# Kernel tuning notes

Measured on AMD Instinct MI355X. Metric: run time of the kernel, lower is better.

Reference implementation:

```python
import jax, jax.numpy as jnp
import numpy as np

ALPHA, GAMMA = 0.25, 2.0
EPS_CLS, EPS_DICE = 1e-8, 1e-5


def box_cxcywh_to_xyxy(b):
    cx, cy, w, h = b[..., 0], b[..., 1], b[..., 2], b[..., 3]
    return jnp.stack([cx - 0.5 * w, cy - 0.5 * h, cx + 0.5 * w, cy + 0.5 * h], axis=-1)


def generalized_box_iou(b1, b2):
    # b1: [N,4], b2: [T,4] in xyxy -> [N,T]
    area1 = (b1[:, 2] - b1[:, 0]) * (b1[:, 3] - b1[:, 1])
    area2 = (b2[:, 2] - b2[:, 0]) * (b2[:, 3] - b2[:, 1])
    lt = jnp.maximum(b1[:, None, :2], b2[None, :, :2])
    rb = jnp.minimum(b1[:, None, 2:], b2[None, :, 2:])
    wh = jnp.clip(rb - lt, 0.0)
    inter = wh[..., 0] * wh[..., 1]
    union = area1[:, None] + area2[None, :] - inter
    iou = inter / union
    lt_e = jnp.minimum(b1[:, None, :2], b2[None, :, :2])
    rb_e = jnp.maximum(b1[:, None, 2:], b2[None, :, 2:])
    wh_e = jnp.clip(rb_e - lt_e, 0.0)
    area_e = wh_e[..., 0] * wh_e[..., 1]
    return iou - (area_e - union) / area_e


def masks_to_boxes(masks):
    # DETR util: masks [N,H,W] (any float; nonzero treated as 'on') -> xyxy [N,4]
    n, h, w = masks.shape
    x = jnp.arange(w, dtype=masks.dtype)
    y = jnp.arange(h, dtype=masks.dtype)
    nz = masks != 0
    x_mask = masks * x[None, None, :]
    x_max = x_mask.reshape(n, -1).max(-1)
    x_min = jnp.where(nz, x_mask, 1e8).reshape(n, -1).min(-1)
    y_mask = masks * y[None, :, None]
    y_max = y_mask.reshape(n, -1).max(-1)
    y_min = jnp.where(nz, y_mask, 1e8).reshape(n, -1).min(-1)
    return jnp.stack([x_min, y_min, x_max, y_max], axis=1)


def setup_inputs() -> dict:
    key = jax.random.key(0)
    k1, k2, k3, k4, k5, k6 = jax.random.split(key, 6)
    return {
        'pred_logits': jax.random.normal(k1, (2, 300, 91), dtype=jnp.float32),
        'pred_boxes': jax.random.uniform(k2, (2, 300, 4), dtype=jnp.float32),
        'pred_masks': jax.random.normal(k3, (2, 300, 256, 256), dtype=jnp.float32),
        'tgt_boxes': jax.random.uniform(k4, (60, 4), dtype=jnp.float32),
        'tgt_ids': jax.random.randint(k5, (60,), 0, 91, dtype=jnp.int64) if jax.config.jax_enable_x64 else jax.random.randint(k5, (60,), 0, 91).astype(jnp.int32),
        'tgt_masks': jax.random.randint(k6, (60, 256, 256), 0, 2, dtype=jnp.int32),
    }


def reference(pred_logits, pred_boxes, pred_masks, tgt_boxes, tgt_ids, tgt_masks):
    bs, Q, C = pred_logits.shape
    N = bs * Q
    tgt_masks_f = tgt_masks.astype(pred_masks.dtype)

    # --- focal classification cost ---
    out_prob = jax.nn.sigmoid(pred_logits.reshape(N, C))
    neg_cc = (1 - ALPHA) * out_prob ** GAMMA * -jnp.log(1 - out_prob + EPS_CLS)
    pos_cc = ALPHA * (1 - out_prob) ** GAMMA * -jnp.log(out_prob + EPS_CLS)
    cost_class = pos_cc[:, tgt_ids] - neg_cc[:, tgt_ids]  # [N,T]

    # --- L1 box cost (cdist p=1) ---
    out_bbox = pred_boxes.reshape(N, 4)
    cost_bbox = jnp.abs(out_bbox[:, None, :] - tgt_boxes[None, :, :]).sum(-1)

    # --- GIoU box cost ---
    cost_giou = -generalized_box_iou(box_cxcywh_to_xyxy(out_bbox),
                                     box_cxcywh_to_xyxy(tgt_boxes))

    # --- GIoU on mask-derived boxes (faithful to original, incl. cxcywh conversion) ---
    out_mask = pred_masks.reshape(N, pred_masks.shape[2], pred_masks.shape[3])
    cost_giou_m2b = -generalized_box_iou(
        box_cxcywh_to_xyxy(masks_to_boxes(out_mask)),
        box_cxcywh_to_xyxy(masks_to_boxes(tgt_masks_f)))

    # --- pairwise dice cost: batched matmul instead of the O(N*T) python loop ---
    HW = out_mask.shape[1] * out_mask.shape[2]
    p = jax.nn.sigmoid(out_mask).reshape(N, HW)      # [N,HW]
    t = tgt_masks_f.reshape(tgt_masks_f.shape[0], HW)  # [T,HW] binary
    inter = p @ t.T                                   # [N,T]
    union = p.sum(1)[:, None] + t.sum(1)[None, :]
    cost_mask_dice = 1.0 - (2 * inter + EPS_DICE) / (union + EPS_DICE)

    # --- pairwise focal cost; exact closed form for binary targets:
    # focal(i,j) = mean_px[ t*pos_px + (1-t)*neg_px ]
    pos_px = ALPHA * (1 - p) ** GAMMA * -jnp.log(p)
    neg_px = (1 - ALPHA) * p ** GAMMA * -jnp.log(1 - p)
    cost_mask_focal = (pos_px @ t.T + neg_px.sum(1)[:, None] - neg_px @ t.T) / HW

    Cmat = (cost_bbox + cost_class + cost_giou +
            cost_giou_m2b + cost_mask_dice + cost_mask_focal)
    return Cmat.reshape(bs, Q, -1)
```

## Files before the change

### kernel.cpp

```cpp
#include <hip/hip_runtime.h>
#include <math.h>

#define HW    65536
#define TNUM  60
#define NPRED 600
#define NCLS  91
#define PS    32
#define NTIL  38

typedef float f32x4 __attribute__((ext_vector_type(4)));
typedef short s16x8 __attribute__((ext_vector_type(8)));

__global__ void hm_tgt_stats(const int* __restrict__ tm, float* __restrict__ tstat) {
    int j = blockIdx.x >> 3, chunk = blockIdx.x & 7;
    int tid = threadIdx.x;
    const int* row = tm + (size_t)j * HW + chunk * 8192;
    float cnt = 0.f, xmax = -INFINITY, ymax = -INFINITY, xmin = INFINITY, ymin = INFINITY;
    for (int i = tid; i < 8192; i += 256) {
        int pix = chunk * 8192 + i;
        float t = (float)row[i];
        float xf = (float)(pix & 255), yf = (float)(pix >> 8);
        float xm = t * xf, ym = t * yf;
        cnt += t;
        xmax = fmaxf(xmax, xm); ymax = fmaxf(ymax, ym);
        bool nz = (t != 0.f);
        xmin = fminf(xmin, nz ? xm : 1e8f);
        ymin = fminf(ymin, nz ? ym : 1e8f);
    }
#pragma unroll
    for (int o = 1; o < 64; o <<= 1) {
        cnt += __shfl_xor(cnt, o);
        xmax = fmaxf(xmax, __shfl_xor(xmax, o));
        ymax = fmaxf(ymax, __shfl_xor(ymax, o));
        xmin = fminf(xmin, __shfl_xor(xmin, o));
        ymin = fminf(ymin, __shfl_xor(ymin, o));
    }
    __shared__ float s[5][4];
    int w = tid >> 6;
    if ((tid & 63) == 0) { s[0][w]=cnt; s[1][w]=xmin; s[2][w]=ymin; s[3][w]=xmax; s[4][w]=ymax; }
    __syncthreads();
    if (tid == 0) {
        float* o = tstat + (size_t)(j * 8 + chunk) * 5;
        o[0] = s[0][0]+s[0][1]+s[0][2]+s[0][3];
        o[1] = fminf(fminf(s[1][0],s[1][1]),fminf(s[1][2],s[1][3]));
        o[2] = fminf(fminf(s[2][0],s[2][1]),fminf(s[2][2],s[2][3]));
        o[3] = fmaxf(fmaxf(s[3][0],s[3][1]),fmaxf(s[3][2],s[3][3]));
        o[4] = fmaxf(fmaxf(s[4][0],s[4][1]),fmaxf(s[4][2],s[4][3]));
    }
}

__global__ void hm_build_tpack(const int* __restrict__ tm, unsigned short* __restrict__ tp) {
    int bid = blockIdx.x;
    int j = bid >> 8, chunk = bid & 255;
    int pix = chunk * 256 + threadIdx.x;
    unsigned short v = 0;
    if (j < TNUM) v = (tm[(size_t)j * HW + pix] != 0) ? (unsigned short)0x3F80 : (unsigned short)0;
    size_t idx = ((size_t)(pix >> 5) * 64 + j) * 32 + (size_t)((pix >> 3) & 3) * 8 + (pix & 7);
    tp[idx] = v;
}

__device__ inline void pix_proc(float x, int e, float xfb, float yf,
                                __bf16* P, __bf16* F,
                                float& sp, float& sn,
                                float& xM, float& yM, float& xm, float& ym) {
    float ex = __expf(x);
    float opex = 1.f + ex;
    float p = __fdividef(ex, opex);
    float spx = __logf(opex);
    float spmx = spx - x;
    float om = 1.f - p;
    float pos = (om * om) * (0.25f * spmx);
    float neg = (p * p) * (0.75f * spx);
    sp += p; sn += neg;
    float xf = xfb + (float)e;
    float xmsk = x * xf, ymsk = x * yf;
    xM = fmaxf(xM, xmsk); yM = fmaxf(yM, ymsk);
    bool nz = (x != 0.f);
    xm = fminf(xm, nz ? xmsk : 1e8f);
    ym = fminf(ym, nz ? ymsk : 1e8f);
    P[e] = (__bf16)p;
    F[e] = (__bf16)(pos - neg);
}

__launch_bounds__(256, 4)
__global__ void hm_heavy(const float* __restrict__ pm, const unsigned short* __restrict__ tp,
                         float* __restrict__ dots, float* __restrict__ stats) {
    int id = blockIdx.x;
    int xcd = id & 7, q = id >> 3;
    int ntile = q % NTIL, ps = xcd + 8 * (q / NTIL);
    int bl = ntile * PS + ps;
    int tid = threadIdx.x, w = tid >> 6, l = tid & 63, g = l >> 4, c = l & 15;
    int n0 = ntile * 16;
    int row = min(n0 + c, NPRED - 1);
    const float* A = pm + (size_t)row * HW;
    const s16x8* tpv = (const s16x8*)tp;
    int pb = ps * 2048 + w * 512;

    f32x4 acc[4][2];
#pragma unroll
    for (int nt = 0; nt < 4; ++nt)
#pragma unroll
        for (int m = 0; m < 2; ++m) acc[nt][m] = (f32x4)0.f;

    float sp = 0.f, sn = 0.f;
    float xM = -INFINITY, yM = -INFINITY, xm = INFINITY, ym = INFINITY;

#pragma unroll 2
    for (int step = 0; step < 16; ++step) {
        int k0 = pb + step * 32;
        int kk = k0 + g * 8;
        float4 aa = *(const float4*)(A + kk);
        float4 ab = *(const float4*)(A + kk + 4);
        float yf = (float)(kk >> 8);
        float xfb = (float)(kk & 255);

        union { __bf16 h[8]; s16x8 v; } P, F;
        float x[8] = {aa.x, aa.y, aa.z, aa.w, ab.x, ab.y, ab.z, ab.w};
#pragma unroll
        for (int e = 0; e < 8; ++e)
            pix_proc(x[e], e, xfb, yf, P.h, F.h, sp, sn, xM, yM, xm, ym);

        int bbase = (k0 >> 5) * 256 + c * 4 + g;
#pragma unroll
        for (int nt = 0; nt < 4; ++nt) {
            s16x8 bf = tpv[bbase + nt * 64];
            acc[nt][0] = __builtin_amdgcn_mfma_f32_16x16x32_bf16(P.v, bf, acc[nt][0], 0, 0, 0);
            acc[nt][1] = __builtin_amdgcn_mfma_f32_16x16x32_bf16(F.v, bf, acc[nt][1], 0, 0, 0);
        }
    }

#pragma unroll
    for (int o = 16; o <= 32; o <<= 1) {
        sp += __shfl_xor(sp, o); sn += __shfl_xor(sn, o);
        xM = fmaxf(xM, __shfl_xor(xM, o)); yM = fmaxf(yM, __shfl_xor(yM, o));
        xm = fminf(xm, __shfl_xor(xm, o)); ym = fminf(ym, __shfl_xor(ym, o));
    }
    if (l < 16) {
        float* so = stats + ((size_t)((bl * 4 + w) * 16 + l)) * 6;
        so[0] = sp; so[1] = sn; so[2] = xM; so[3] = yM; so[4] = xm; so[5] = ym;
    }

    __shared__ float ldsD[4][32][64];
#pragma unroll
    for (int nt = 0; nt < 4; ++nt)
#pragma unroll
        for (int m = 0; m < 2; ++m)
#pragma unroll
            for (int r = 0; r < 4; ++r)
                ldsD[w][(nt * 2 + m) * 4 + r][l] = acc[nt][m][r];
    __syncthreads();

    for (int idx = tid; idx < 2048; idx += 256) {
        int mat = idx >> 10, rl = (idx >> 6) & 15, col = idx & 63;
        int gg = rl >> 2, rg = rl & 3;
        int nt = col >> 4, cc = col & 15;
        int lane = gg * 16 + cc;
        int off = (nt * 2 + mat) * 4 + rg;
        float s = ldsD[0][off][lane] + ldsD[1][off][lane] + ldsD[2][off][lane] + ldsD[3][off][lane];
        dots[(size_t)bl * 2048 + idx] = s;
    }
}

__global__ void hm_pred_reduce(const float* __restrict__ stats, float* __restrict__ pstat) {
    int n = blockIdx.x;
    int l = threadIdx.x;
    int ntile = n >> 4, r = n & 15;
    const float* s0 = stats + ((size_t)(ntile * 128 + l) * 16 + r) * 6;
    const float* s1 = stats + ((size_t)(ntile * 128 + l + 64) * 16 + r) * 6;
    float v0 = s0[0] + s1[0];
    float v1 = s0[1] + s1[1];
    float v2 = fmaxf(s0[2], s1[2]);
    float v3 = fmaxf(s0[3], s1[3]);
    float v4 = fminf(s0[4], s1[4]);
    float v5 = fminf(s0[5], s1[5]);
#pragma unroll
    for (int o = 1; o < 64; o <<= 1) {
        v0 += __shfl_xor(v0, o); v1 += __shfl_xor(v1, o);
        v2 = fmaxf(v2, __shfl_xor(v2, o)); v3 = fmaxf(v3, __shfl_xor(v3, o));
        v4 = fminf(v4, __shfl_xor(v4, o)); v5 = fminf(v5, __shfl_xor(v5, o));
    }
    if (l == 0) {
        float* o = pstat + (size_t)n * 6;
        o[0] = v0; o[1] = v1; o[2] = v2; o[3] = v3; o[4] = v4; o[5] = v5;
    }
}

__device__ inline float giou2(float ax0, float ay0, float ax1, float ay1,
                              float bx0, float by0, float bx1, float by1) {
    float area1 = (ax1 - ax0) * (ay1 - ay0);
    float area2 = (bx1 - bx0) * (by1 - by0);
    float ltx = fmaxf(ax0, bx0), lty = fmaxf(ay0, by0);
    float rbx = fminf(ax1, bx1), rby = fminf(ay1, by1);
    float iw = fmaxf(rbx - ltx, 0.f), ih = fmaxf(rby - lty, 0.f);
    float inter = iw * ih;
    float uni = area1 + area2 - inter;
    float iou = inter / uni;
    float ex0 = fminf(ax0, bx0), ey0 = fminf(ay0, by0);
    float ex1 = fmaxf(ax1, bx1), ey1 = fmaxf(ay1, by1);
    float ew = fmaxf(ex1 - ex0, 0.f), eh = fmaxf(ey1 - ey0, 0.f);
    float ae = ew * eh;
    return iou - (ae - uni) / ae;
}

__device__ inline float giou_cxcywh(float acx, float acy, float aw, float ah,
                                    float bcx, float bcy, float bw, float bh) {
    return giou2(acx - 0.5f * aw, acy - 0.5f * ah, acx + 0.5f * aw, acy + 0.5f * ah,
                 bcx - 0.5f * bw, bcy - 0.5f * bh, bcx + 0.5f * bw, bcy + 0.5f * bh);
}

__global__ void hm_combine(const float* __restrict__ pred_logits,
                           const float* __restrict__ pred_boxes,
                           const float* __restrict__ tgt_boxes,
                           const int* __restrict__ tgt_ids,
                           const float* __restrict__ dots,
                           const float* __restrict__ pstat,
                           const float* __restrict__ tstat,
                           float* __restrict__ out) {
    int idx = blockIdx.x * blockDim.x + threadIdx.x;
    if (idx >= NPRED * TNUM) return;
    int n = idx / TNUM, j = idx % TNUM;
    int ntile = n >> 4, r = n & 15;

    const float* db = dots + (size_t)ntile * PS * 2048 + r * 64 + j;
    float dp = 0.f, df = 0.f;
#pragma unroll
    for (int ps = 0; ps < PS; ++ps) {
        dp += db[ps * 2048];
        df += db[ps * 2048 + 1024];
    }

    float tcnt = 0.f, txm = INFINITY, tym = INFINITY, txM = -INFINITY, tyM = -INFINITY;
#pragma unroll
    for (int k = 0; k < 8; ++k) {
        const float* tb = tstat + (size_t)(j * 8 + k) * 5;
        tcnt += tb[0];
        txm = fminf(txm, tb[1]); tym = fminf(tym, tb[2]);
        txM = fmaxf(txM, tb[3]); tyM = fmaxf(tyM, tb[4]);
    }

    const float* pp = pstat + (size_t)n * 6;
    float sum_p = pp[0], sum_neg = pp[1];
    float pxM = pp[2], pyM = pp[3], pxm = pp[4], pym = pp[5];

    float4 ob = ((const float4*)pred_boxes)[n];
    float4 tb4 = ((const float4*)tgt_boxes)[j];
    float cbbox = fabsf(ob.x - tb4.x) + fabsf(ob.y - tb4.y) + fabsf(ob.z - tb4.z) + fabsf(ob.w - tb4.w);

    float cgiou = -giou_cxcywh(ob.x, ob.y, ob.z, ob.w, tb4.x, tb4.y, tb4.z, tb4.w);

    int id = tgt_ids[j];
    float lg = pred_logits[(size_t)n * NCLS + id];
    float e = __expf(lg);
    float pr = __fdividef(e, 1.f + e);
    float poscc = 0.25f * (1.f - pr) * (1.f - pr) * (-__logf(pr + 1e-8f));
    float negcc = 0.75f * pr * pr * (-__logf(1.f - pr + 1e-8f));
    float cclass = poscc - negcc;

    float cm2b = -giou_cxcywh(pxm, pym, pxM, pyM, txm, tym, txM, tyM);

    float un = sum_p + tcnt;
    float cdice = 1.f - (2.f * dp + 1e-5f) / (un + 1e-5f);

    float cfocal = (df + sum_neg) * (1.0f / (float)HW);

    out[idx] = cbbox + cclass + cgiou + cm2b + cdice + cfocal;
}

extern "C" void kernel_launch(void* const* d_in, const int* in_sizes, int n_in,
                              void* d_out, int out_size, void* d_ws, size_t ws_size,
                              hipStream_t stream) {
    const float* pred_logits = (const float*)d_in[0];
    const float* pred_boxes  = (const float*)d_in[1];
    const float* pred_masks  = (const float*)d_in[2];
    const float* tgt_boxes   = (const float*)d_in[3];
    const int*   tgt_ids     = (const int*)d_in[4];
    const int*   tgt_masks   = (const int*)d_in[5];
    float* out = (float*)d_out;

    char* wsb = (char*)d_ws;
    unsigned short* tpack = (unsigned short*)wsb;
    float* dots  = (float*)(wsb + 8388608);
    float* stats = (float*)(wsb + 18350080);
    float* pstat = (float*)(wsb + 20217856);
    float* tstat = (float*)(wsb + 20232256);

    hipLaunchKernelGGL(hm_tgt_stats, dim3(TNUM * 8), dim3(256), 0, stream, tgt_masks, tstat);
    hipLaunchKernelGGL(hm_build_tpack, dim3(64 * 256), dim3(256), 0, stream, tgt_masks, tpack);
    hipLaunchKernelGGL(hm_heavy, dim3(NTIL * PS), dim3(256), 0, stream, pred_masks, tpack, dots, stats);
    hipLaunchKernelGGL(hm_pred_reduce, dim3(NPRED), dim3(64), 0, stream, stats, pstat);
    hipLaunchKernelGGL(hm_combine, dim3((NPRED * TNUM + 255) / 256), dim3(256), 0, stream,
                       pred_logits, pred_boxes, tgt_boxes, tgt_ids, dots, pstat, tstat, out);
}
```

Before: 94.07 us.

## Split heavy kernel per-wave over K, drop LDS reduction, store partial dots in fp16

The heavy kernel is restructured so each 128-thread block holds two waves working on different 16-row tiles, and each wave owns its own 512-pixel K slice (128 slices instead of 32). This removes the in-block LDS cross-wave reduction and its __syncthreads. Partial dot products are written directly as packed half2 (dice and focal together). The combine kernel now sums 128 partials per output instead of 32. This trades LDS traffic and sync for more partial-sum memory traffic, and fp16 storage of partial sums loses precision.

```diff
diff --git a/kernel.cpp b/kernel.cpp
--- a/kernel.cpp
+++ b/kernel.cpp
@@ -1,12 +1,13 @@
 #include <hip/hip_runtime.h>
+#include <hip/hip_fp16.h>
 #include <math.h>
 
 #define HW    65536
 #define TNUM  60
 #define NPRED 600
 #define NCLS  91
-#define PS    32
-#define NTIL  38
+#define PS    128
+#define RTP   20
 
 typedef float f32x4 __attribute__((ext_vector_type(4)));
 typedef short s16x8 __attribute__((ext_vector_type(8)));
@@ -82,19 +83,19 @@
     F[e] = (__bf16)(pos - neg);
 }
 
-__launch_bounds__(256, 4)
+__launch_bounds__(128, 8)
 __global__ void hm_heavy(const float* __restrict__ pm, const unsigned short* __restrict__ tp,
-                         float* __restrict__ dots, float* __restrict__ stats) {
+                         __half2* __restrict__ dots, float* __restrict__ stats) {
     int id = blockIdx.x;
     int xcd = id & 7, q = id >> 3;
-    int ntile = q % NTIL, ps = xcd + 8 * (q / NTIL);
-    int bl = ntile * PS + ps;
+    int rtp = q % RTP, psg = q / RTP;
+    int ps = xcd + 8 * psg;
     int tid = threadIdx.x, w = tid >> 6, l = tid & 63, g = l >> 4, c = l & 15;
-    int n0 = ntile * 16;
-    int row = min(n0 + c, NPRED - 1);
+    int rt = rtp * 2 + w;
+    int row = min(rt * 16 + c, NPRED - 1);
     const float* A = pm + (size_t)row * HW;
     const s16x8* tpv = (const s16x8*)tp;
-    int pb = ps * 2048 + w * 512;
+    int pb = ps * 512;
 
     f32x4 acc[4][2];
 #pragma unroll
@@ -136,37 +137,28 @@
         xm = fminf(xm, __shfl_xor(xm, o)); ym = fminf(ym, __shfl_xor(ym, o));
     }
     if (l < 16) {
-        float* so = stats + ((size_t)((bl * 4 + w) * 16 + l)) * 6;
+        float* so = stats + ((size_t)(rt * PS + ps) * 16 + l) * 6;
         so[0] = sp; so[1] = sn; so[2] = xM; so[3] = yM; so[4] = xm; so[5] = ym;
     }
 
-    __shared__ float ldsD[4][32][64];
+    size_t dbase = (size_t)(rt * PS + ps) * 1024;
 #pragma unroll
     for (int nt = 0; nt < 4; ++nt)
 #pragma unroll
-        for (int m = 0; m < 2; ++m)
-#pragma unroll
-            for (int r = 0; r < 4; ++r)
-                ldsD[w][(nt * 2 + m) * 4 + r][l] = acc[nt][m][r];
-    __syncthreads();
-
-    for (int idx = tid; idx < 2048; idx += 256) {
-        int mat = idx >> 10, rl = (idx >> 6) & 15, col = idx & 63;
-        int gg = rl >> 2, rg = rl & 3;
-        int nt = col >> 4, cc = col & 15;
-        int lane = gg * 16 + cc;
-        int off = (nt * 2 + mat) * 4 + rg;
-        float s = ldsD[0][off][lane] + ldsD[1][off][lane] + ldsD[2][off][lane] + ldsD[3][off][lane];
-        dots[(size_t)bl * 2048 + idx] = s;
-    }
+        for (int r = 0; r < 4; ++r) {
+            __half2 h;
+            h.x = __float2half_rn(acc[nt][0][r]);
+            h.y = __float2half_rn(acc[nt][1][r]);
+            dots[dbase + (size_t)((g * 4 + r) * 64 + nt * 16 + c)] = h;
+        }
 }
 
 __global__ void hm_pred_reduce(const float* __restrict__ stats, float* __restrict__ pstat) {
     int n = blockIdx.x;
     int l = threadIdx.x;
-    int ntile = n >> 4, r = n & 15;
-    const float* s0 = stats + ((size_t)(ntile * 128 + l) * 16 + r) * 6;
-    const float* s1 = stats + ((size_t)(ntile * 128 + l + 64) * 16 + r) * 6;
+    int rt = n >> 4, r = n & 15;
+    const float* s0 = stats + ((size_t)(rt * PS + l) * 16 + r) * 6;
+    const float* s1 = stats + ((size_t)(rt * PS + l + 64) * 16 + r) * 6;
     float v0 = s0[0] + s1[0];
     float v1 = s0[1] + s1[1];
     float v2 = fmaxf(s0[2], s1[2]);
@@ -212,21 +204,22 @@
                            const float* __restrict__ pred_boxes,
                            const float* __restrict__ tgt_boxes,
                            const int* __restrict__ tgt_ids,
-                           const float* __restrict__ dots,
+                           const __half2* __restrict__ dots,
                            const float* __restrict__ pstat,
                            const float* __restrict__ tstat,
                            float* __restrict__ out) {
     int idx = blockIdx.x * blockDim.x + threadIdx.x;
     if (idx >= NPRED * TNUM) return;
     int n = idx / TNUM, j = idx % TNUM;
-    int ntile = n >> 4, r = n & 15;
-
-    const float* db = dots + (size_t)ntile * PS * 2048 + r * 64 + j;
+    int rt = n >> 4, r = n & 15;
+
+    const __half2* db = dots + (size_t)rt * PS * 1024 + r * 64 + j;
     float dp = 0.f, df = 0.f;
-#pragma unroll
+#pragma unroll 8
     for (int ps = 0; ps < PS; ++ps) {
-        dp += db[ps * 2048];
-        df += db[ps * 2048 + 1024];
+        __half2 v = db[(size_t)ps * 1024];
+        dp += __half2float(v.x);
+        df += __half2float(v.y);
     }
 
     float tcnt = 0.f, txm = INFINITY, tym = INFINITY, txM = -INFINITY, tyM = -INFINITY;
@@ -279,14 +272,14 @@
 
     char* wsb = (char*)d_ws;
     unsigned short* tpack = (unsigned short*)wsb;
-    float* dots  = (float*)(wsb + 8388608);
-    float* stats = (float*)(wsb + 18350080);
-    float* pstat = (float*)(wsb + 20217856);
-    float* tstat = (float*)(wsb + 20232256);
+    __half2* dots = (__half2*)(wsb + 8388608);
+    float* stats  = (float*)(wsb + 29360128);
+    float* pstat  = (float*)(wsb + 31326208);
+    float* tstat  = (float*)(wsb + 31340608);
 
     hipLaunchKernelGGL(hm_tgt_stats, dim3(TNUM * 8), dim3(256), 0, stream, tgt_masks, tstat);
     hipLaunchKernelGGL(hm_build_tpack, dim3(64 * 256), dim3(256), 0, stream, tgt_masks, tpack);
-    hipLaunchKernelGGL(hm_heavy, dim3(NTIL * PS), dim3(256), 0, stream, pred_masks, tpack, dots, stats);
+    hipLaunchKernelGGL(hm_heavy, dim3(RTP * PS), dim3(128), 0, stream, pred_masks, tpack, dots, stats);
     hipLaunchKernelGGL(hm_pred_reduce, dim3(NPRED), dim3(64), 0, stream, stats, pstat);
     hipLaunchKernelGGL(hm_combine, dim3((NPRED * TNUM + 255) / 256), dim3(256), 0, stream,
                        pred_logits, pred_boxes, tgt_boxes, tgt_ids, dots, pstat, tstat, out);
```

Result: slower. 335.2 us (+256.3%).

## Double split-K partitions, raise occupancy, reduce heavy-kernel stats in-block

Applied to the files above, without the earlier changes.

Splits the pixel dimension into twice as many partitions, so each block handles half as many pixels and twice as many blocks are launched. Launch bounds rise to 6 waves-groups per CU, and the LDS staging buffer is halved by reducing the two accumulator matrices one after the other. Per-wave stats are now combined inside the block, and the sigmoid's divide is replaced by a hardware reciprocal. The cost is twice as many partial dot-product results written to and read back from global memory, plus a few extra barriers.

```diff
diff --git a/kernel.cpp b/kernel.cpp
--- a/kernel.cpp
+++ b/kernel.cpp
@@ -5,7 +5,7 @@
 #define TNUM  60
 #define NPRED 600
 #define NCLS  91
-#define PS    32
+#define PS    64
 #define NTIL  38
 
 typedef float f32x4 __attribute__((ext_vector_type(4)));
@@ -65,10 +65,10 @@
                                 float& xM, float& yM, float& xm, float& ym) {
     float ex = __expf(x);
     float opex = 1.f + ex;
-    float p = __fdividef(ex, opex);
+    float om = __builtin_amdgcn_rcpf(opex);
+    float p = 1.f - om;
     float spx = __logf(opex);
     float spmx = spx - x;
-    float om = 1.f - p;
     float pos = (om * om) * (0.25f * spmx);
     float neg = (p * p) * (0.75f * spx);
     sp += p; sn += neg;
@@ -82,19 +82,20 @@
     F[e] = (__bf16)(pos - neg);
 }
 
-__launch_bounds__(256, 4)
+__launch_bounds__(256, 6)
 __global__ void hm_heavy(const float* __restrict__ pm, const unsigned short* __restrict__ tp,
                          float* __restrict__ dots, float* __restrict__ stats) {
     int id = blockIdx.x;
     int xcd = id & 7, q = id >> 3;
-    int ntile = q % NTIL, ps = xcd + 8 * (q / NTIL);
+    int ntile = q % NTIL, psg = q / NTIL;
+    int ps = xcd + 8 * psg;
     int bl = ntile * PS + ps;
     int tid = threadIdx.x, w = tid >> 6, l = tid & 63, g = l >> 4, c = l & 15;
     int n0 = ntile * 16;
     int row = min(n0 + c, NPRED - 1);
     const float* A = pm + (size_t)row * HW;
     const s16x8* tpv = (const s16x8*)tp;
-    int pb = ps * 2048 + w * 512;
+    int pb = ps * 1024 + w * 256;
 
     f32x4 acc[4][2];
 #pragma unroll
@@ -106,7 +107,7 @@
     float xM = -INFINITY, yM = -INFINITY, xm = INFINITY, ym = INFINITY;
 
 #pragma unroll 2
-    for (int step = 0; step < 16; ++step) {
+    for (int step = 0; step < 8; ++step) {
         int k0 = pb + step * 32;
         int kk = k0 + g * 8;
         float4 aa = *(const float4*)(A + kk);
@@ -135,29 +136,55 @@
         xM = fmaxf(xM, __shfl_xor(xM, o)); yM = fmaxf(yM, __shfl_xor(yM, o));
         xm = fminf(xm, __shfl_xor(xm, o)); ym = fminf(ym, __shfl_xor(ym, o));
     }
-    if (l < 16) {
-        float* so = stats + ((size_t)((bl * 4 + w) * 16 + l)) * 6;
-        so[0] = sp; so[1] = sn; so[2] = xM; so[3] = yM; so[4] = xm; so[5] = ym;
-    }
-
-    __shared__ float ldsD[4][32][64];
+
+    __shared__ float ldsD[4][16][64];
 #pragma unroll
     for (int nt = 0; nt < 4; ++nt)
 #pragma unroll
-        for (int m = 0; m < 2; ++m)
-#pragma unroll
-            for (int r = 0; r < 4; ++r)
-                ldsD[w][(nt * 2 + m) * 4 + r][l] = acc[nt][m][r];
-    __syncthreads();
-
-    for (int idx = tid; idx < 2048; idx += 256) {
-        int mat = idx >> 10, rl = (idx >> 6) & 15, col = idx & 63;
+        for (int r = 0; r < 4; ++r)
+            ldsD[w][nt * 4 + r][l] = acc[nt][0][r];
+    __syncthreads();
+    for (int idx = tid; idx < 1024; idx += 256) {
+        int rl = (idx >> 6) & 15, col = idx & 63;
         int gg = rl >> 2, rg = rl & 3;
         int nt = col >> 4, cc = col & 15;
         int lane = gg * 16 + cc;
-        int off = (nt * 2 + mat) * 4 + rg;
+        int off = nt * 4 + rg;
         float s = ldsD[0][off][lane] + ldsD[1][off][lane] + ldsD[2][off][lane] + ldsD[3][off][lane];
         dots[(size_t)bl * 2048 + idx] = s;
+    }
+    __syncthreads();
+#pragma unroll
+    for (int nt = 0; nt < 4; ++nt)
+#pragma unroll
+        for (int r = 0; r < 4; ++r)
+            ldsD[w][nt * 4 + r][l] = acc[nt][1][r];
+    __syncthreads();
+    for (int idx = tid; idx < 1024; idx += 256) {
+        int rl = (idx >> 6) & 15, col = idx & 63;
+        int gg = rl >> 2, rg = rl & 3;
+        int nt = col >> 4, cc = col & 15;
+        int lane = gg * 16 + cc;
+        int off = nt * 4 + rg;
+        float s = ldsD[0][off][lane] + ldsD[1][off][lane] + ldsD[2][off][lane] + ldsD[3][off][lane];
+        dots[(size_t)bl * 2048 + 1024 + idx] = s;
+    }
+    __syncthreads();
+    float* ldsS = (float*)ldsD;
+    if (l < 16) {
+        float* so = ldsS + w * 96 + l * 6;
+        so[0] = sp; so[1] = sn; so[2] = xM; so[3] = yM; so[4] = xm; so[5] = ym;
+    }
+    __syncthreads();
+    if (tid < 96) {
+        int rr = tid / 6, s = tid % 6;
+        float a0 = ldsS[0 * 96 + rr * 6 + s], a1 = ldsS[1 * 96 + rr * 6 + s];
+        float a2 = ldsS[2 * 96 + rr * 6 + s], a3 = ldsS[3 * 96 + rr * 6 + s];
+        float r;
+        if (s < 2)      r = a0 + a1 + a2 + a3;
+        else if (s < 4) r = fmaxf(fmaxf(a0, a1), fmaxf(a2, a3));
+        else            r = fminf(fminf(a0, a1), fminf(a2, a3));
+        stats[(size_t)(bl * 16 + rr) * 6 + s] = r;
     }
 }
 
@@ -165,14 +192,8 @@
     int n = blockIdx.x;
     int l = threadIdx.x;
     int ntile = n >> 4, r = n & 15;
-    const float* s0 = stats + ((size_t)(ntile * 128 + l) * 16 + r) * 6;
-    const float* s1 = stats + ((size_t)(ntile * 128 + l + 64) * 16 + r) * 6;
-    float v0 = s0[0] + s1[0];
-    float v1 = s0[1] + s1[1];
-    float v2 = fmaxf(s0[2], s1[2]);
-    float v3 = fmaxf(s0[3], s1[3]);
-    float v4 = fminf(s0[4], s1[4]);
-    float v5 = fminf(s0[5], s1[5]);
+    const float* sb = stats + ((size_t)((ntile * PS + l) * 16 + r)) * 6;
+    float v0 = sb[0], v1 = sb[1], v2 = sb[2], v3 = sb[3], v4 = sb[4], v5 = sb[5];
 #pragma unroll
     for (int o = 1; o < 64; o <<= 1) {
         v0 += __shfl_xor(v0, o); v1 += __shfl_xor(v1, o);
@@ -280,9 +301,9 @@
     char* wsb = (char*)d_ws;
     unsigned short* tpack = (unsigned short*)wsb;
     float* dots  = (float*)(wsb + 8388608);
-    float* stats = (float*)(wsb + 18350080);
-    float* pstat = (float*)(wsb + 20217856);
-    float* tstat = (float*)(wsb + 20232256);
+    float* stats = (float*)(wsb + 28311552);
+    float* pstat = (float*)(wsb + 29245440);
+    float* tstat = (float*)(wsb + 29259840);
 
     hipLaunchKernelGGL(hm_tgt_stats, dim3(TNUM * 8), dim3(256), 0, stream, tgt_masks, tstat);
     hipLaunchKernelGGL(hm_build_tpack, dim3(64 * 256), dim3(256), 0, stream, tgt_masks, tpack);
```

Result: slower. 221.3 us (+135.3%).
